# Performance work log

Hardware: AMD Instinct MI355X
Metric: run time of the kernel (lower is better)

Reference implementation:

```python
import jax, jax.numpy as jnp
from jax import lax
import numpy as np

V, D, H, E, L, B = 512, 128, 64, 4, 60, 4096
ADJ = 184  # ((180 + 7) // 8) * 8


def setup_inputs() -> dict:
    key = jax.random.key(0)
    it = iter(jax.random.split(key, 64))

    def nrm(shape, s=0.05):
        return jax.random.normal(next(it), shape, dtype=jnp.float32) * s

    x = jax.random.randint(next(it), (B, L), 0, V, dtype=jnp.int32)
    inp = {"x": x, "emb": nrm((V, D), 0.02).at[0].set(0.0)}  # padding_idx=0 row zero
    for d in ("f", "r"):
        inp[f"w_ih_{d}"] = nrm((4 * H, D)); inp[f"w_hh_{d}"] = nrm((4 * H, H))
        inp[f"b_ih_{d}"] = nrm((4 * H,)); inp[f"b_hh_{d}"] = nrm((4 * H,))
    for p, i_, h_, o_ in (("e", 1, 16, 8), ("l", 1, 16, 8), ("c", V, 32, 16), ("p", 6, 24, 12), ("x", 4, 16, 8)):
        inp[f"{p}_w1"] = nrm((h_, i_)); inp[f"{p}_b1"] = nrm((h_,))
        inp[f"{p}_w2"] = nrm((o_, h_)); inp[f"{p}_b2"] = nrm((o_,))
    inp["fp_w"] = nrm((ADJ, 180)); inp["fp_b"] = nrm((ADJ,))
    inp["attn_w"] = nrm((3 * ADJ, ADJ)); inp["attn_b"] = nrm((3 * ADJ,))
    inp["out_w"] = nrm((ADJ, ADJ)); inp["out_b"] = nrm((ADJ,))
    for i, (o_, i_) in enumerate(((128, ADJ), (64, 128), (32, 64), (E, 32)), 1):
        inp[f"g_w{i}"] = nrm((o_, i_)); inp[f"g_b{i}"] = nrm((o_,))
    return inp


def _mlp2(h, w1, b1, w2, b2):
    return jnp.maximum(h @ w1.T + b1, 0.0) @ w2.T + b2


def _lstm_final(xe, w_ih, w_hh, b_ih, b_hh):
    # torch LSTM gate order i, f, g, o; returns final hidden state [B, H]
    xg = jnp.einsum('bld,gd->blg', xe, w_ih) + b_ih
    h0 = jnp.zeros((xe.shape[0], H), xe.dtype)

    def step(carry, g_t):
        h, c = carry
        g = g_t + h @ w_hh.T + b_hh
        i, f, gg, o = jnp.split(g, 4, axis=-1)
        c = jax.nn.sigmoid(f) * c + jax.nn.sigmoid(i) * jnp.tanh(gg)
        h = jax.nn.sigmoid(o) * jnp.tanh(c)
        return (h, c), None

    (h, _), _ = lax.scan(step, (h0, h0), jnp.swapaxes(xg, 0, 1))
    return h


def _sequence_stats(x):
    # Fully vectorized equivalent of the per-sequence python loops
    f32 = jnp.float32
    mask = x != 0
    vlen = mask.sum(1)                                       # [B]
    vlenf = jnp.maximum(vlen, 1).astype(f32)
    pos = jnp.arange(L)
    # per-row histogram over valid tokens (torch.bincount of valid_seq)
    counts = jnp.zeros((B, V), f32).at[jnp.arange(B)[:, None], x].add(mask.astype(f32))
    probs = counts / jnp.maximum(counts.sum(1, keepdims=True), 1.0)
    entropy = -jnp.sum(probs * jnp.log(probs + 1e-8), axis=1)
    entropy = jnp.where(vlen > 1, entropy, 0.0)
    char_dist = counts / vlenf[:, None]
    # compact valid tokens to the front (torch: seq[seq != 0]), stable argsort
    order = jnp.argsort((~mask).astype(jnp.int32), axis=1)
    cseq = jnp.take_along_axis(x, order, axis=1)
    cseq = jnp.where(pos[None] < vlen[:, None], cseq, 0)
    a, b = cseq[:, :-1], cseq[:, 1:]
    pairmask = pos[: L - 1][None] < (vlen - 1)[:, None]
    den1 = jnp.maximum(vlen - 1, 1).astype(f32)
    repeat = ((a == b) & pairmask).sum(1) / den1
    inc = ((b > a) & pairmask).sum(1) / den1
    dec = ((b < a) & pairmask).sum(1) / den1
    m2 = pos[: L - 2][None] < (vlen - 2)[:, None]
    per = ((cseq[:, :-2] == cseq[:, 2:]) & m2).sum(1) / jnp.maximum(vlen - 2, 1)
    per = jnp.where(vlen >= 4, per, 0.0)
    diversity = (counts > 0).sum(1) / vlenf
    # longest run of equal consecutive tokens via cummax of reset positions
    eq = jnp.concatenate([jnp.zeros((B, 1), bool), (cseq[:, 1:] == cseq[:, :-1]) & (pos[1:][None] < vlen[:, None])], 1)
    lastreset = lax.cummax(jnp.where(eq, -1, pos[None]), axis=1)
    runlen = pos[None] - lastreset + 1
    max_rep = jnp.where(pos[None] < vlen[:, None], runlen, 0).max(1) / vlenf
    pattern = jnp.stack([repeat, inc, dec, per, diversity, max_rep], 1).astype(f32)
    pattern = jnp.where((vlen > 1)[:, None], pattern, 0.0)
    # unique bigrams: sort pair codes, count distinct valid codes
    codes = jnp.where(pairmask, a * V + b, -1)
    s = jnp.sort(codes, axis=1)
    prevc = jnp.concatenate([jnp.full((B, 1), -2, s.dtype), s[:, :-1]], 1)
    comp_ratio = ((s != prevc) & (s >= 0)).sum(1) / den1
    info_density = entropy / jnp.log(jnp.maximum(vlen, 2).astype(f32))
    # local complexity: mean over sliding windows of (#unique / w), w = min(5, len//2)
    wsel = jnp.minimum(5, vlen // 2)
    local = jnp.zeros((B,), f32)
    for w in (2, 3, 4, 5):
        nwin = L - w + 1
        sh = [cseq[:, k:k + nwin] for k in range(w)]
        u = jnp.ones((B, nwin), f32)
        for k in range(1, w):
            isnew = jnp.ones((B, nwin), bool)
            for m in range(k):
                isnew = isnew & (sh[k] != sh[m])
            u = u + isnew
        winmask = pos[:nwin][None] < (vlen - w + 1)[:, None]
        lc = (u * winmask).sum(1) / w / jnp.maximum(vlen - w + 1, 1)
        local = jnp.where(wsel == w, lc, local)
    trans = 1.0 - repeat  # transitions/(len-1) == 1 - repeat_ratio
    complexity = jnp.stack([comp_ratio, info_density, local, trans], 1).astype(f32)
    complexity = jnp.where((vlen > 1)[:, None], complexity, 0.0)
    return entropy, vlen, char_dist, pattern, complexity


def reference(x, emb, w_ih_f, w_hh_f, b_ih_f, b_hh_f, w_ih_r, w_hh_r, b_ih_r, b_hh_r, e_w1, e_b1, e_w2, e_b2, l_w1, l_b1, l_w2, l_b2, c_w1, c_b1, c_w2, c_b2, p_w1, p_b1, p_w2, p_b2, x_w1, x_b1, x_w2, x_b2, fp_w, fp_b, attn_w, attn_b, out_w, out_b, g_w1, g_b1, g_w2, g_b2, g_w3, g_b3, g_w4, g_b4):
    entropy, vlen, char_dist, pattern, complexity = _sequence_stats(x)
    xe = emb[x]                                               # [B, L, D]
    h_f = _lstm_final(xe, w_ih_f, w_hh_f, b_ih_f, b_hh_f)
    h_r = _lstm_final(xe[:, ::-1], w_ih_r, w_hh_r, b_ih_r, b_hh_r)
    feats = jnp.concatenate([
        h_f, h_r,
        _mlp2((entropy / 4.0)[:, None], e_w1, e_b1, e_w2, e_b2),
        _mlp2((vlen.astype(jnp.float32) / 60.0)[:, None], l_w1, l_b1, l_w2, l_b2),
        _mlp2(char_dist, c_w1, c_b1, c_w2, c_b2),
        _mlp2(pattern, p_w1, p_b1, p_w2, p_b2),
        _mlp2(complexity, x_w1, x_b1, x_w2, x_b2),
    ], axis=1)                                                # [B, 180]
    f = feats @ fp_w.T + fp_b                                 # [B, 184]
    # MultiheadAttention with seq_len == 1: softmax over a single key is 1,
    # so attended = out_proj(v_proj(f)) exactly (q/k projections cancel).
    wv, bv = attn_w[2 * ADJ:], attn_b[2 * ADJ:]
    attended = (f @ wv.T + bv) @ out_w.T + out_b
    h = jnp.maximum(attended @ g_w1.T + g_b1, 0.0)
    h = jnp.maximum(h @ g_w2.T + g_b2, 0.0)
    h = jnp.maximum(h @ g_w3.T + g_b3, 0.0)
    logits = h @ g_w4.T + g_b4
    return jax.nn.softmax(logits, axis=-1)  # eval path (training=False)
```

## Files before the change

### kernel.cpp

```cpp
#include <hip/hip_runtime.h>

#define BATCH 4096
#define SEQL  60
#define VOC   512
#define EMBD  128
#define HID   64
#define GATES 256
#define ADJ   184

typedef __attribute__((ext_vector_type(8))) short short8;
typedef __attribute__((ext_vector_type(4))) float f32x4;
typedef __attribute__((ext_vector_type(4))) unsigned short u16x4;

#define L2E  1.4426950408889634f
#define L2E2 2.8853900817779268f

__device__ __forceinline__ float ex2(float x) {
#if __has_builtin(__builtin_amdgcn_exp2f)
  return __builtin_amdgcn_exp2f(x);
#else
  return exp2f(x);
#endif
}
__device__ __forceinline__ unsigned short f2bf_rne(float f) {
  unsigned int u = __float_as_uint(f);
  unsigned int r = (u + 0x7fffu + ((u >> 16) & 1u)) >> 16;
  return (unsigned short)r;
}
__device__ __forceinline__ unsigned short f2bf(float f) {
  return (unsigned short)((__float_as_uint(f) + 0x8000u) >> 16);
}
__device__ __forceinline__ float dot4(float4 a, float4 b, float acc) {
  acc = fmaf(a.x, b.x, acc); acc = fmaf(a.y, b.y, acc);
  acc = fmaf(a.z, b.z, acc); acc = fmaf(a.w, b.w, acc);
  return acc;
}
__device__ __forceinline__ float wsumf(float v) {
  #pragma unroll
  for (int s = 32; s > 0; s >>= 1) v += __shfl_xor(v, s, 64);
  return v;
}
__device__ __forceinline__ int wsumi(int v) {
  #pragma unroll
  for (int s = 32; s > 0; s >>= 1) v += __shfl_xor(v, s, 64);
  return v;
}
__device__ __forceinline__ int wmaxi(int v) {
  #pragma unroll
  for (int s = 32; s > 0; s >>= 1) v = max(v, __shfl_xor(v, s, 64));
  return v;
}

__global__ __launch_bounds__(256) void k_prep(
    const int* __restrict__ x,
    const float* __restrict__ emb,
    const float* __restrict__ wih_f, const float* __restrict__ bif, const float* __restrict__ bhf,
    const float* __restrict__ wih_r, const float* __restrict__ bir, const float* __restrict__ bhr,
    const float* __restrict__ whh_f, const float* __restrict__ whh_r,
    const float* __restrict__ g_w1, const float* __restrict__ g_b1,
    const float* __restrict__ out_w, const float* __restrict__ out_b,
    const float* __restrict__ attn_w, const float* __restrict__ attn_b,
    const float* __restrict__ fp_w, const float* __restrict__ fp_b,
    const float* __restrict__ g_w2, const float* __restrict__ g_w3,
    const float* __restrict__ g_w4, const float* __restrict__ c_w1,
    float* __restrict__ G_f, float* __restrict__ G_r,
    unsigned short* __restrict__ Wfrag,
    float* __restrict__ A, float* __restrict__ avb,
    float* __restrict__ Bp, float* __restrict__ vb,
    float* __restrict__ g_w2t, float* __restrict__ g_w3t, float* __restrict__ g_w4t,
    float* __restrict__ c_w1t,
    float* __restrict__ ent_o, float* __restrict__ vlen_o,
    float* __restrict__ pat_o, float* __restrict__ cpx_o) {
  __shared__ unsigned int cnt[4][512];
  __shared__ unsigned short q[4][68];
  const int bid = blockIdx.x;
  const int tid = threadIdx.x;

  if (bid < 128) {
    const int dir = bid >> 6;
    const int rem = bid & 63;
    const int v0 = (rem >> 2) * 32;
    const int j0 = (rem & 3) * 64;
    const float* W = dir ? wih_r : wih_f;
    const float* bi = dir ? bir : bif;
    const float* bh = dir ? bhr : bhf;
    float* G = dir ? G_r : G_f;
    const int vp = tid >> 4;
    const int jq = tid & 15;
    const int v = v0 + vp * 2;
    const int j = j0 + jq * 4;
    const int gg = j >> 6;
    const int u0 = j & 63;
    const float sc = (gg == 2) ? L2E2 : L2E;

    const float4* E0 = (const float4*)(emb + (size_t)v * 128);
    const float4* E1 = (const float4*)(emb + (size_t)(v + 1) * 128);
    const float4* W0 = (const float4*)(W + (size_t)j * 128);
    const float4* W1 = (const float4*)(W + (size_t)(j + 1) * 128);
    const float4* W2 = (const float4*)(W + (size_t)(j + 2) * 128);
    const float4* W3 = (const float4*)(W + (size_t)(j + 3) * 128);

    float a00 = 0.f, a01 = 0.f, a02 = 0.f, a03 = 0.f;
    float a10 = 0.f, a11 = 0.f, a12 = 0.f, a13 = 0.f;
    #pragma unroll 4
    for (int d4 = 0; d4 < 32; d4++) {
      float4 e0 = E0[d4], e1 = E1[d4];
      float4 w0 = W0[d4], w1 = W1[d4], w2 = W2[d4], w3 = W3[d4];
      a00 = dot4(e0, w0, a00); a01 = dot4(e0, w1, a01);
      a02 = dot4(e0, w2, a02); a03 = dot4(e0, w3, a03);
      a10 = dot4(e1, w0, a10); a11 = dot4(e1, w1, a11);
      a12 = dot4(e1, w2, a12); a13 = dot4(e1, w3, a13);
    }
    float b0v = bi[j] + bh[j], b1v = bi[j + 1] + bh[j + 1];
    float b2v = bi[j + 2] + bh[j + 2], b3v = bi[j + 3] + bh[j + 3];
    float* g0 = G + (size_t)v * 256 + u0 * 4 + gg;
    g0[0]  = (a00 + b0v) * sc; g0[4]  = (a01 + b1v) * sc;
    g0[8]  = (a02 + b2v) * sc; g0[12] = (a03 + b3v) * sc;
    float* g1 = g0 + 256;
    g1[0]  = (a10 + b0v) * sc; g1[4]  = (a11 + b1v) * sc;
    g1[8]  = (a12 + b2v) * sc; g1[12] = (a13 + b3v) * sc;
  } else if (bid < 144) {
    const int id = (bid - 128) * 256 + tid;
    const int lane = id & 63;
    const int fc = id >> 6;
    const int c = fc & 1;
    const int gg = (fc >> 1) & 3;
    const int w = (fc >> 3) & 3;
    const int dir = fc >> 5;
    const float* whh = dir ? whh_r : whh_f;
    const float sc = (gg == 2) ? L2E2 : L2E;
    const int n = gg * 64 + w * 16 + (lane & 15);
    const int kb = c * 32 + (lane >> 4) * 8;
    unsigned short* o = Wfrag + (size_t)id * 8;
    #pragma unroll
    for (int j = 0; j < 8; j++) o[j] = f2bf_rne(whh[n * 64 + kb + j] * sc);
  } else if (bid < 272) {
    const int i = bid - 144;
    const int j = tid;
    const float* g1r = g_w1 + (size_t)i * ADJ;
    if (j < ADJ) {
      float a0 = 0.f, a1 = 0.f, a2 = 0.f, a3 = 0.f;
      for (int k = 0; k < ADJ; k += 4) {
        a0 = fmaf(g1r[k],     out_w[(size_t)(k)     * ADJ + j], a0);
        a1 = fmaf(g1r[k + 1], out_w[(size_t)(k + 1) * ADJ + j], a1);
        a2 = fmaf(g1r[k + 2], out_w[(size_t)(k + 2) * ADJ + j], a2);
        a3 = fmaf(g1r[k + 3], out_w[(size_t)(k + 3) * ADJ + j], a3);
      }
      A[(size_t)i * ADJ + j] = (a0 + a1) + (a2 + a3);
    } else if (j == ADJ) {
      float a0 = 0.f;
      for (int k = 0; k < ADJ; k++) a0 = fmaf(g1r[k], out_b[k], a0);
      avb[i] = a0 + g_b1[i];
    }
  } else if (bid < 456) {
    const int k = bid - 272;
    const int j = tid;
    const float* wvr = attn_w + (size_t)(2 * ADJ + k) * ADJ;
    if (j < 180) {
      float a0 = 0.f, a1 = 0.f, a2 = 0.f, a3 = 0.f;
      for (int m = 0; m < ADJ; m += 4) {
        a0 = fmaf(wvr[m],     fp_w[(size_t)(m)     * 180 + j], a0);
        a1 = fmaf(wvr[m + 1], fp_w[(size_t)(m + 1) * 180 + j], a1);
        a2 = fmaf(wvr[m + 2], fp_w[(size_t)(m + 2) * 180 + j], a2);
        a3 = fmaf(wvr[m + 3], fp_w[(size_t)(m + 3) * 180 + j], a3);
      }
      Bp[(size_t)k * 180 + j] = (a0 + a1) + (a2 + a3);
    } else if (j == 180) {
      float a0 = 0.f;
      for (int m = 0; m < ADJ; m++) a0 = fmaf(wvr[m], fp_b[m], a0);
      vb[k] = a0 + attn_b[2 * ADJ + k];
    }
  } else if (bid == 456) {
    for (int i = tid; i < 64 * 128; i += 256) {
      int o = i >> 7, k = i & 127;
      g_w2t[k * 64 + o] = g_w2[i];
    }
    for (int i = tid; i < 32 * 64; i += 256) {
      int o = i >> 6, k = i & 63;
      g_w3t[k * 32 + o] = g_w3[i];
    }
    if (tid < 128) {
      int o = tid >> 5, k = tid & 31;
      g_w4t[k * 4 + o] = g_w4[tid];
    }
  } else if (bid < 465) {
    const int base = (bid - 457) * 2048;
    for (int i = tid; i < 2048; i += 256) {
      int idx = base + i;
      int o = idx >> 9, k = idx & 511;
      c_w1t[k * 32 + o] = k ? c_w1[o * 512 + k] : 0.f;
    }
  } else {
    const int lane = tid & 63;
    const int wid = tid >> 6;
    const int row = (bid - 465) * 4 + wid;
    unsigned int* cr = cnt[wid];
    unsigned short* qr = q[wid];

    for (int i = lane; i < 512; i += 64) cr[i] = 0u;
    qr[lane] = 0;
    if (lane < 4) qr[64 + lane] = 0;
    int v = (lane < 60) ? x[row * 60 + lane] : 0;
    bool act = (v != 0);
    unsigned long long amask = __ballot(act);
    int n = __popcll(amask);
    __syncthreads();
    if (act) {
      int pos = __popcll(amask & ((1ull << lane) - 1ull));
      qr[pos] = (unsigned short)v;
      atomicAdd(&cr[v], 1u);
    }
    __syncthreads();

    float vlenf = (float)(n >= 1 ? n : 1);
    float inv = 1.f / vlenf;

    float ent = 0.f; int distinct = 0;
    #pragma unroll
    for (int j = 0; j < 8; j++) {
      unsigned int c = cr[lane + j * 64];
      if (c) {
        distinct++;
        float p = (float)c * inv;
        ent -= p * __logf(p + 1e-8f);
      }
    }
    ent = wsumf(ent);
    distinct = wsumi(distinct);

    int a = qr[lane], b = qr[lane + 1], c2 = qr[lane + 2];
    bool v1 = (lane + 1 < n);
    bool v2 = (lane + 2 < n);
    int rep  = __popcll(__ballot(v1 && (a == b)));
    int incs = __popcll(__ballot(v1 && (b > a)));
    int decs = __popcll(__ballot(v1 && (b < a)));
    int per2 = __popcll(__ballot(v2 && (a == c2)));

    int prev = (lane > 0) ? (int)qr[lane - 1] : -1;
    bool isst = (lane < n) && (lane == 0 || a != prev);
    unsigned long long smask = __ballot(isst);
    int len = 0;
    if (isst) {
      unsigned long long hi = (lane < 63) ? (smask >> (lane + 1)) : 0ull;
      int next = hi ? (lane + __ffsll((unsigned long long)hi)) : n;
      len = next - lane;
    }
    int maxrun = wmaxi(len);

    int code = v1 ? (a * VOC + b) : -1;
    int unique = v1 ? 1 : 0;
    #pragma unroll 1
    for (int j = 0; j < 58; j++) {
      int cj = __shfl(code, j, 64);
      if (j < lane && cj == code) unique = 0;
    }
    int dc = __popcll(__ballot(unique != 0));

    int wl = n >> 1; if (wl > 5) wl = 5;
    float local = 0.f;
    if (wl >= 2) {
      bool pv = (lane + wl <= n);
      int u = 0;
      if (pv) {
        int t0 = qr[lane], t1 = qr[lane + 1], t2 = qr[lane + 2];
        int t3 = qr[lane + 3], t4 = qr[lane + 4];
        u = 1;
        u += (t1 != t0);
        if (wl >= 3) u += (int)((t2 != t1) && (t2 != t0));
        if (wl >= 4) u += (int)((t3 != t2) && (t3 != t1) && (t3 != t0));
        if (wl >= 5) u += (int)((t4 != t3) && (t4 != t2) && (t4 != t1) && (t4 != t0));
      }
      int usum = wsumi(u);
      int denw = n - wl + 1; if (denw < 1) denw = 1;
      local = (float)usum / (float)wl / (float)denw;
    }

    float den1 = (float)((n - 1) >= 1 ? (n - 1) : 1);
    float repeat = (float)rep / den1;
    float per = (n >= 4) ? (float)per2 / (float)((n - 2) >= 1 ? (n - 2) : 1) : 0.f;
    float entz = (n > 1) ? ent : 0.f;
    float z = (n > 1) ? 1.f : 0.f;

    if (lane == 0) {
      ent_o[row] = entz;
      vlen_o[row] = (float)n;
      pat_o[row * 6 + 0] = repeat * z;
      pat_o[row * 6 + 1] = (float)incs / den1 * z;
      pat_o[row * 6 + 2] = (float)decs / den1 * z;
      pat_o[row * 6 + 3] = per * z;
      pat_o[row * 6 + 4] = (float)distinct * inv * z;
      pat_o[row * 6 + 5] = (float)maxrun * inv * z;
      cpx_o[row * 4 + 0] = (float)dc / den1 * z;
      cpx_o[row * 4 + 1] = entz / __logf((float)(n >= 2 ? n : 2)) * z;
      cpx_o[row * 4 + 2] = local * z;
      cpx_o[row * 4 + 3] = (1.f - repeat) * z;
    }
  }
}

#define LSTM_BAR()                                                             \
  do {                                                                         \
    asm volatile("s_waitcnt lgkmcnt(0)" ::: "memory");                         \
    __builtin_amdgcn_s_barrier();                                              \
    __builtin_amdgcn_sched_barrier(0);                                         \
  } while (0)

#define LSTM_STEP(T, CUR, NXT)                                                 \
  {                                                                            \
    const unsigned short* hb = hbuf[(T) & 1];                                  \
    short8 hf0 = *(const short8*)(hb + rdoff);                                 \
    short8 hf1 = *(const short8*)(hb + rdoff + 32);                            \
    if ((T) < 59) {                                                            \
      int tsn = dir ? (58 - (T)) : ((T) + 1);                                  \
      const char* gp = Gb2 + tokoff[tsn * 16 + ln];                            \
      NXT[0] = *(const float4*)(gp);                                           \
      NXT[1] = *(const float4*)(gp + 16);                                      \
      NXT[2] = *(const float4*)(gp + 32);                                      \
      NXT[3] = *(const float4*)(gp + 48);                                      \
    }                                                                          \
    f32x4 z0 = {0.f, 0.f, 0.f, 0.f};                                           \
    f32x4 acc0 = z0, acc1 = z0, acc2 = z0, acc3 = z0;                          \
    acc0 = __builtin_amdgcn_mfma_f32_16x16x32_bf16(bfr[0][0], hf0, acc0, 0, 0, 0); \
    acc1 = __builtin_amdgcn_mfma_f32_16x16x32_bf16(bfr[1][0], hf0, acc1, 0, 0, 0); \
    acc2 = __builtin_amdgcn_mfma_f32_16x16x32_bf16(bfr[2][0], hf0, acc2, 0, 0, 0); \
    acc3 = __builtin_amdgcn_mfma_f32_16x16x32_bf16(bfr[3][0], hf0, acc3, 0, 0, 0); \
    acc0 = __builtin_amdgcn_mfma_f32_16x16x32_bf16(bfr[0][1], hf1, acc0, 0, 0, 0); \
    acc1 = __builtin_amdgcn_mfma_f32_16x16x32_bf16(bfr[1][1], hf1, acc1, 0, 0, 0); \
    acc2 = __builtin_amdgcn_mfma_f32_16x16x32_bf16(bfr[2][1], hf1, acc2, 0, 0, 0); \
    acc3 = __builtin_amdgcn_mfma_f32_16x16x32_bf16(bfr[3][1], hf1, acc3, 0, 0, 0); \
    unsigned short* hw = hbuf[((T) + 1) & 1];                                  \
    unsigned short hh[4];                                                      \
    _Pragma("unroll")                                                          \
    for (int r = 0; r < 4; r++) {                                              \
      float gi = acc0[r] + CUR[r].x;                                           \
      float gf = acc1[r] + CUR[r].y;                                           \
      float gc = acc2[r] + CUR[r].z;                                           \
      float go = acc3[r] + CUR[r].w;                                           \
      float Ef = ex2(-gf);                                                     \
      float E1 = ex2(-gi);                                                     \
      float E2 = ex2(gc);                                                      \
      float sf = __builtin_amdgcn_rcpf(1.f + Ef);                              \
      float p  = (E2 - 1.f) * __builtin_amdgcn_rcpf((1.f + E1) * (E2 + 1.f));  \
      float cn = fmaf(sf, cst[r], p);                                          \
      cst[r] = cn;                                                             \
      float E3 = ex2(-go);                                                     \
      float E4 = ex2(fminf(L2E2 * cn, 126.f));                                 \
      float h  = (E4 - 1.f) * __builtin_amdgcn_rcpf((1.f + E3) * (E4 + 1.f));  \
      hv[r] = h;                                                               \
      hh[r] = f2bf(h);                                                         \
    }                                                                          \
    u16x4 hvv = {hh[0], hh[1], hh[2], hh[3]};                                  \
    *(u16x4*)(hw + wroff) = hvv;                                               \
    if ((T) == 59) {                                                           \
      float4 o4; o4.x = hv[0]; o4.y = hv[1]; o4.z = hv[2]; o4.w = hv[3];       \
      *(float4*)(hop) = o4;                                                    \
    }                                                                          \
    LSTM_BAR();                                                                \
  }

__global__ __launch_bounds__(256) void k_main(
    const int* __restrict__ x,
    const float* __restrict__ G_f, const float* __restrict__ G_r,
    const unsigned short* __restrict__ Wfrag,
    const float* __restrict__ A, const float* __restrict__ avb,
    const float* __restrict__ Bp, const float* __restrict__ vb,
    float* __restrict__ C1t, float* __restrict__ c1b,
    float* __restrict__ hf_o, float* __restrict__ hr_o) {
  __shared__ __align__(16) unsigned short hbuf[2][16 * 72];
  __shared__ __align__(16) unsigned int tokoff[60 * 16];
  const int bid = blockIdx.x;
  const int tid = threadIdx.x;

  if (bid < 512) {
    const int lane = tid & 63;
    const int w = tid >> 6;
    const int dir = bid >> 8;
    const int blk = bid & 255;
    const int b0 = blk << 4;
    const float* G = dir ? G_r : G_f;
    float* ho = dir ? hr_o : hf_o;

    for (int i = tid; i < 960; i += 256) {
      int r = i / 60, t = i - r * 60;
      tokoff[t * 16 + r] = ((unsigned int)x[(size_t)(b0 + r) * 60 + t]) << 10;
    }
    for (int i = tid; i < 16 * 72; i += 256) hbuf[0][i] = 0;

    short8 bfr[4][2];
    #pragma unroll
    for (int gg = 0; gg < 4; gg++)
      #pragma unroll
      for (int c = 0; c < 2; c++) {
        int idx = (((dir * 4 + w) * 4 + gg) * 2 + c) * 64 + lane;
        bfr[gg][c] = *(const short8*)(Wfrag + (size_t)idx * 8);
      }

    const int kg = lane >> 4;
    const int ln = lane & 15;
    const int ub2 = w * 16 + kg * 4;
    const int rdoff = ln * 72 + kg * 8;
    const int wroff = ln * 72 + ub2;
    const char* Gb2 = (const char*)G + (size_t)ub2 * 16;
    float* hop = ho + (size_t)(b0 + ln) * 64 + ub2;
    float cst[4] = {0.f, 0.f, 0.f, 0.f};
    float4 gvA[4], gvB[4];
    float hv[4];

    __syncthreads();

    {
      int ts0 = dir ? 59 : 0;
      const char* gp = Gb2 + tokoff[ts0 * 16 + ln];
      gvA[0] = *(const float4*)(gp);
      gvA[1] = *(const float4*)(gp + 16);
      gvA[2] = *(const float4*)(gp + 32);
      gvA[3] = *(const float4*)(gp + 48);
    }

    #pragma unroll 1
    for (int tt = 0; tt < 30; tt++) {
      const int t0 = tt * 2, t1 = tt * 2 + 1;
      LSTM_STEP(t0, gvA, gvB)
      LSTM_STEP(t1, gvB, gvA)
    }
  } else {
    const int i = bid - 512, j = tid;
    const float* Ar = A + (size_t)i * ADJ;
    if (j < 180) {
      float a0 = 0.f, a1 = 0.f, a2 = 0.f, a3 = 0.f;
      for (int k = 0; k < ADJ; k += 4) {
        a0 = fmaf(Ar[k],     Bp[(size_t)(k)     * 180 + j], a0);
        a1 = fmaf(Ar[k + 1], Bp[(size_t)(k + 1) * 180 + j], a1);
        a2 = fmaf(Ar[k + 2], Bp[(size_t)(k + 2) * 180 + j], a2);
        a3 = fmaf(Ar[k + 3], Bp[(size_t)(k + 3) * 180 + j], a3);
      }
      C1t[(size_t)j * 128 + i] = (a0 + a1) + (a2 + a3);
    } else if (j == 180) {
      float a0 = 0.f;
      for (int k = 0; k < ADJ; k++) a0 = fmaf(Ar[k], vb[k], a0);
      c1b[i] = a0 + avb[i];
    }
  }
}

#define FSTR 192

__global__ __launch_bounds__(256) void k_head(
    const int* __restrict__ x,
    const float* __restrict__ hf, const float* __restrict__ hr,
    const float* __restrict__ ent, const float* __restrict__ vlen,
    const float* __restrict__ pat, const float* __restrict__ cpx,
    const float* __restrict__ e_w1, const float* __restrict__ e_b1,
    const float* __restrict__ e_w2, const float* __restrict__ e_b2,
    const float* __restrict__ l_w1, const float* __restrict__ l_b1,
    const float* __restrict__ l_w2, const float* __restrict__ l_b2,
    const float* __restrict__ c_w1t, const float* __restrict__ c_b1,
    const float* __restrict__ c_w2, const float* __restrict__ c_b2,
    const float* __restrict__ p_w1, const float* __restrict__ p_b1,
    const float* __restrict__ p_w2, const float* __restrict__ p_b2,
    const float* __restrict__ x_w1, const float* __restrict__ x_b1,
    const float* __restrict__ x_w2, const float* __restrict__ x_b2,
    const float* __restrict__ C1t, const float* __restrict__ c1b,
    const float* __restrict__ g_w2t, const float* __restrict__ g_b2,
    const float* __restrict__ g_w3t, const float* __restrict__ g_b3,
    const float* __restrict__ g_w4t, const float* __restrict__ g_b4,
    float* __restrict__ out) {
  __shared__ float feat[8 * FSTR];
  __shared__ unsigned short tk[8 * 64];
  __shared__ float h1[8 * 128];
  __shared__ float h2[8 * 64];
  __shared__ float h3[8 * 32];
  __shared__ float h1c[8 * 33];
  __shared__ float lg[32];
  const int tid = threadIdx.x;
  const int b0 = blockIdx.x * 8;

  if (tid < 128) {
    int r = tid >> 4, c = tid & 15;
    float4 vv = ((const float4*)(hf + (size_t)(b0 + r) * 64))[c];
    *(float4*)(feat + r * FSTR + c * 4) = vv;
  } else {
    int t = tid - 128;
    int r = t >> 4, c = t & 15;
    float4 vv = ((const float4*)(hr + (size_t)(b0 + r) * 64))[c];
    *(float4*)(feat + r * FSTR + 64 + c * 4) = vv;
  }
  for (int i = tid; i < 480; i += 256) {
    int r = i / 60, t = i - r * 60;
    tk[r * 64 + t] = (unsigned short)x[(size_t)(b0 + r) * 60 + t];
  }
  __syncthreads();
  {
    int o = tid & 31, r = tid >> 5;
    const unsigned short* tkr = tk + r * 64;
    float a0 = 0.f, a1 = 0.f, a2 = 0.f, a3 = 0.f;
    #pragma unroll 5
    for (int t = 0; t < 60; t += 4) {
      int t0 = tkr[t], t1 = tkr[t + 1], t2 = tkr[t + 2], t3 = tkr[t + 3];
      a0 += c_w1t[t0 * 32 + o];
      a1 += c_w1t[t1 * 32 + o];
      a2 += c_w1t[t2 * 32 + o];
      a3 += c_w1t[t3 * 32 + o];
    }
    float invv = __builtin_amdgcn_rcpf(fmaxf(vlen[b0 + r], 1.f));
    h1c[r * 33 + o] = fmaxf(((a0 + a1) + (a2 + a3)) * invv + c_b1[o], 0.f);
  }
  __syncthreads();
  if (tid < 32) {
    const int m = tid & 3, r = tid >> 2, b = b0 + r;
    float tt[24];
    if (m == 0) {
      float ein = ent[b] * 0.25f;
      #pragma unroll
      for (int o = 0; o < 16; o++) tt[o] = fmaxf(e_w1[o] * ein + e_b1[o], 0.f);
      #pragma unroll
      for (int o = 0; o < 8; o++) {
        float a = e_b2[o];
        #pragma unroll
        for (int k = 0; k < 16; k++) a = fmaf(e_w2[o * 16 + k], tt[k], a);
        feat[r * FSTR + 128 + o] = a;
      }
    } else if (m == 1) {
      float lin = vlen[b] * (1.f / 60.f);
      #pragma unroll
      for (int o = 0; o < 16; o++) tt[o] = fmaxf(l_w1[o] * lin + l_b1[o], 0.f);
      #pragma unroll
      for (int o = 0; o < 8; o++) {
        float a = l_b2[o];
        #pragma unroll
        for (int k = 0; k < 16; k++) a = fmaf(l_w2[o * 16 + k], tt[k], a);
        feat[r * FSTR + 136 + o] = a;
      }
    } else if (m == 2) {
      float pin[6];
      #pragma unroll
      for (int k = 0; k < 6; k++) pin[k] = pat[b * 6 + k];
      #pragma unroll
      for (int o = 0; o < 24; o++) {
        float a = p_b1[o];
        #pragma unroll
        for (int k = 0; k < 6; k++) a = fmaf(p_w1[o * 6 + k], pin[k], a);
        tt[o] = fmaxf(a, 0.f);
      }
      #pragma unroll
      for (int o = 0; o < 12; o++) {
        float a = p_b2[o];
        #pragma unroll
        for (int k = 0; k < 24; k++) a = fmaf(p_w2[o * 24 + k], tt[k], a);
        feat[r * FSTR + 160 + o] = a;
      }
    } else {
      float xin[4];
      #pragma unroll
      for (int k = 0; k < 4; k++) xin[k] = cpx[b * 4 + k];
      #pragma unroll
      for (int o = 0; o < 16; o++) {
        float a = x_b1[o];
        #pragma unroll
        for (int k = 0; k < 4; k++) a = fmaf(x_w1[o * 4 + k], xin[k], a);
        tt[o] = fmaxf(a, 0.f);
      }
      #pragma unroll
      for (int o = 0; o < 8; o++) {
        float a = x_b2[o];
        #pragma unroll
        for (int k = 0; k < 16; k++) a = fmaf(x_w2[o * 16 + k], tt[k], a);
        feat[r * FSTR + 172 + o] = a;
      }
    }
  } else if (tid >= 64 && tid < 192) {
    int t = tid - 64;
    int r = t >> 4, o = t & 15;
    float a = c_b2[o];
    const float* hh = h1c + r * 33;
    #pragma unroll
    for (int k = 0; k < 32; k++) a = fmaf(c_w2[o * 32 + k], hh[k], a);
    feat[r * FSTR + 144 + o] = a;
  }
  __syncthreads();

  {
    const int o = tid & 127, rg = tid >> 7;
    const float* f0p = feat + (rg * 4 + 0) * FSTR;
    const float* f1p = feat + (rg * 4 + 1) * FSTR;
    const float* f2p = feat + (rg * 4 + 2) * FSTR;
    const float* f3p = feat + (rg * 4 + 3) * FSTR;
    float a0 = 0.f, a1 = 0.f, a2 = 0.f, a3 = 0.f;
    #pragma unroll 3
    for (int k4 = 0; k4 < 45; k4++) {
      float w0 = C1t[(size_t)(k4 * 4 + 0) * 128 + o];
      float w1 = C1t[(size_t)(k4 * 4 + 1) * 128 + o];
      float w2 = C1t[(size_t)(k4 * 4 + 2) * 128 + o];
      float w3 = C1t[(size_t)(k4 * 4 + 3) * 128 + o];
      float4 f0 = *(const float4*)(f0p + k4 * 4);
      float4 f1 = *(const float4*)(f1p + k4 * 4);
      float4 f2 = *(const float4*)(f2p + k4 * 4);
      float4 f3 = *(const float4*)(f3p + k4 * 4);
      a0 = fmaf(w0, f0.x, a0); a0 = fmaf(w1, f0.y, a0);
      a0 = fmaf(w2, f0.z, a0); a0 = fmaf(w3, f0.w, a0);
      a1 = fmaf(w0, f1.x, a1); a1 = fmaf(w1, f1.y, a1);
      a1 = fmaf(w2, f1.z, a1); a1 = fmaf(w3, f1.w, a1);
      a2 = fmaf(w0, f2.x, a2); a2 = fmaf(w1, f2.y, a2);
      a2 = fmaf(w2, f2.z, a2); a2 = fmaf(w3, f2.w, a2);
      a3 = fmaf(w0, f3.x, a3); a3 = fmaf(w1, f3.y, a3);
      a3 = fmaf(w2, f3.z, a3); a3 = fmaf(w3, f3.w, a3);
    }
    float bb = c1b[o];
    h1[(rg * 4 + 0) * 128 + o] = fmaxf(a0 + bb, 0.f);
    h1[(rg * 4 + 1) * 128 + o] = fmaxf(a1 + bb, 0.f);
    h1[(rg * 4 + 2) * 128 + o] = fmaxf(a2 + bb, 0.f);
    h1[(rg * 4 + 3) * 128 + o] = fmaxf(a3 + bb, 0.f);
  }
  __syncthreads();
  {
    const int o = tid & 63, rg = tid >> 6;
    const float* f0p = h1 + (rg * 2 + 0) * 128;
    const float* f1p = h1 + (rg * 2 + 1) * 128;
    float a0 = 0.f, a1 = 0.f;
    #pragma unroll 4
    for (int k4 = 0; k4 < 32; k4++) {
      float w0 = g_w2t[(k4 * 4 + 0) * 64 + o];
      float w1 = g_w2t[(k4 * 4 + 1) * 64 + o];
      float w2 = g_w2t[(k4 * 4 + 2) * 64 + o];
      float w3 = g_w2t[(k4 * 4 + 3) * 64 + o];
      float4 f0 = *(const float4*)(f0p + k4 * 4);
      float4 f1 = *(const float4*)(f1p + k4 * 4);
      a0 = fmaf(w0, f0.x, a0); a0 = fmaf(w1, f0.y, a0);
      a0 = fmaf(w2, f0.z, a0); a0 = fmaf(w3, f0.w, a0);
      a1 = fmaf(w0, f1.x, a1); a1 = fmaf(w1, f1.y, a1);
      a1 = fmaf(w2, f1.z, a1); a1 = fmaf(w3, f1.w, a1);
    }
    float bb = g_b2[o];
    h2[(rg * 2 + 0) * 64 + o] = fmaxf(a0 + bb, 0.f);
    h2[(rg * 2 + 1) * 64 + o] = fmaxf(a1 + bb, 0.f);
  }
  __syncthreads();
  {
    const int o = tid & 31, rg = tid >> 5;
    const float* fp = h2 + rg * 64;
    float a = 0.f;
    #pragma unroll 4
    for (int k4 = 0; k4 < 16; k4++) {
      float w0 = g_w3t[(k4 * 4 + 0) * 32 + o];
      float w1 = g_w3t[(k4 * 4 + 1) * 32 + o];
      float w2 = g_w3t[(k4 * 4 + 2) * 32 + o];
      float w3 = g_w3t[(k4 * 4 + 3) * 32 + o];
      float4 f0 = *(const float4*)(fp + k4 * 4);
      a = fmaf(w0, f0.x, a); a = fmaf(w1, f0.y, a);
      a = fmaf(w2, f0.z, a); a = fmaf(w3, f0.w, a);
    }
    h3[rg * 32 + o] = fmaxf(a + g_b3[o], 0.f);
  }
  __syncthreads();
  if (tid < 32) {
    int r = tid >> 2, o = tid & 3;
    const float* hh = h3 + r * 32;
    float a = g_b4[o];
    #pragma unroll
    for (int k = 0; k < 32; k++) a = fmaf(g_w4t[k * 4 + o], hh[k], a);
    lg[tid] = a;
  }
  __syncthreads();
  if (tid < 8) {
    float l0 = lg[tid * 4 + 0], l1 = lg[tid * 4 + 1];
    float l2 = lg[tid * 4 + 2], l3 = lg[tid * 4 + 3];
    float m = fmaxf(fmaxf(l0, l1), fmaxf(l2, l3));
    float e0 = __expf(l0 - m), e1 = __expf(l1 - m);
    float e2 = __expf(l2 - m), e3 = __expf(l3 - m);
    float is = __builtin_amdgcn_rcpf(e0 + e1 + e2 + e3);
    float4 o4; o4.x = e0 * is; o4.y = e1 * is; o4.z = e2 * is; o4.w = e3 * is;
    *(float4*)(out + (size_t)(b0 + tid) * 4) = o4;
  }
}

extern "C" void kernel_launch(void* const* d_in, const int* in_sizes, int n_in,
                              void* d_out, int out_size, void* d_ws, size_t ws_size,
                              hipStream_t stream) {
  const int*   x     = (const int*)d_in[0];
  const float* emb   = (const float*)d_in[1];
  const float* wih_f = (const float*)d_in[2];
  const float* whh_f = (const float*)d_in[3];
  const float* bih_f = (const float*)d_in[4];
  const float* bhh_f = (const float*)d_in[5];
  const float* wih_r = (const float*)d_in[6];
  const float* whh_r = (const float*)d_in[7];
  const float* bih_r = (const float*)d_in[8];
  const float* bhh_r = (const float*)d_in[9];
  const float* e_w1 = (const float*)d_in[10]; const float* e_b1 = (const float*)d_in[11];
  const float* e_w2 = (const float*)d_in[12]; const float* e_b2 = (const float*)d_in[13];
  const float* l_w1 = (const float*)d_in[14]; const float* l_b1 = (const float*)d_in[15];
  const float* l_w2 = (const float*)d_in[16]; const float* l_b2 = (const float*)d_in[17];
  const float* c_w1 = (const float*)d_in[18]; const float* c_b1 = (const float*)d_in[19];
  const float* c_w2 = (const float*)d_in[20]; const float* c_b2 = (const float*)d_in[21];
  const float* p_w1 = (const float*)d_in[22]; const float* p_b1 = (const float*)d_in[23];
  const float* p_w2 = (const float*)d_in[24]; const float* p_b2 = (const float*)d_in[25];
  const float* x_w1 = (const float*)d_in[26]; const float* x_b1 = (const float*)d_in[27];
  const float* x_w2 = (const float*)d_in[28]; const float* x_b2 = (const float*)d_in[29];
  const float* fp_w = (const float*)d_in[30]; const float* fp_b = (const float*)d_in[31];
  const float* attn_w = (const float*)d_in[32]; const float* attn_b = (const float*)d_in[33];
  const float* out_w = (const float*)d_in[34]; const float* out_b = (const float*)d_in[35];
  const float* g_w1 = (const float*)d_in[36]; const float* g_b1 = (const float*)d_in[37];
  const float* g_w2 = (const float*)d_in[38]; const float* g_b2 = (const float*)d_in[39];
  const float* g_w3 = (const float*)d_in[40]; const float* g_b3 = (const float*)d_in[41];
  const float* g_w4 = (const float*)d_in[42]; const float* g_b4 = (const float*)d_in[43];

  float* ws   = (float*)d_ws;
  float* G_f  = ws;
  float* G_r  = G_f  + 512 * 256;
  float* hfw  = G_r  + 512 * 256;
  float* hrw  = hfw  + BATCH * 64;
  float* entw = hrw  + BATCH * 64;
  float* vlnw = entw + BATCH;
  float* patw = vlnw + BATCH;
  float* cpxw = patw + BATCH * 6;
  float* Aw   = cpxw + BATCH * 4;
  float* avbw = Aw + 128 * ADJ;
  float* Bpw  = avbw + 128;
  float* vbw  = Bpw + ADJ * 180;
  float* C1t  = vbw + ADJ;
  float* c1b  = C1t + 180 * 128;
  float* g2t  = c1b + 128;
  float* g3t  = g2t + 128 * 64;
  float* g4t  = g3t + 64 * 32;
  float* cw1t = g4t + 32 * 4;
  unsigned short* Wfrag = (unsigned short*)(cw1t + 512 * 32);

  k_prep<<<dim3(465 + BATCH / 4), dim3(256), 0, stream>>>(
      x, emb, wih_f, bih_f, bhh_f, wih_r, bih_r, bhh_r, whh_f, whh_r,
      g_w1, g_b1, out_w, out_b, attn_w, attn_b, fp_w, fp_b,
      g_w2, g_w3, g_w4, c_w1,
      G_f, G_r, Wfrag, Aw, avbw, Bpw, vbw, g2t, g3t, g4t, cw1t,
      entw, vlnw, patw, cpxw);
  k_main<<<dim3(640), dim3(256), 0, stream>>>(
      x, G_f, G_r, Wfrag, Aw, avbw, Bpw, vbw, C1t, c1b, hfw, hrw);
  k_head<<<dim3(BATCH / 8), dim3(256), 0, stream>>>(
      x, hfw, hrw, entw, vlnw, patw, cpxw,
      e_w1, e_b1, e_w2, e_b2, l_w1, l_b1, l_w2, l_b2,
      cw1t, c_b1, c_w2, c_b2, p_w1, p_b1, p_w2, p_b2,
      x_w1, x_b1, x_w2, x_b2, C1t, c1b,
      g2t, g_b2, g3t, g_b3, g4t, g_b4,
      (float*)d_out);
}
```

Baseline: 250.2 us.

## Stage LSTM input-gate rows into LDS via async global_load_lds double buffer

Replaces the per-lane register prefetch of the next timestep's precomputed input-gate rows with async global-to-LDS loads (global_load_lds, 16 bytes per lane), double-buffered in shared memory. Each wave fetches whole 1KB token rows coalesced, and lanes then read their gate slices from LDS. The custom lgkmcnt barrier becomes __syncthreads, which also waits on vmcnt, so the loads of the next step must finish before each step's barrier. That can stall the serial recurrence on global latency, and the change also raises LDS use.

```diff
diff --git a/kernel.cpp b/kernel.cpp
--- a/kernel.cpp
+++ b/kernel.cpp
@@ -15,6 +15,8 @@
 #define L2E  1.4426950408889634f
 #define L2E2 2.8853900817779268f
 
+#define GROW 1040
+
 __device__ __forceinline__ float ex2(float x) {
 #if __has_builtin(__builtin_amdgcn_exp2f)
   return __builtin_amdgcn_exp2f(x);
@@ -49,6 +51,11 @@
   #pragma unroll
   for (int s = 32; s > 0; s >>= 1) v = max(v, __shfl_xor(v, s, 64));
   return v;
+}
+__device__ __forceinline__ void gload16(const void* g, void* l) {
+  __builtin_amdgcn_global_load_lds(
+      (const __attribute__((address_space(1))) void*)g,
+      (__attribute__((address_space(3))) void*)l, 16, 0, 0);
 }
 
 __global__ __launch_bounds__(256) void k_prep(
@@ -298,26 +305,26 @@
   }
 }
 
-#define LSTM_BAR()                                                             \
-  do {                                                                         \
-    asm volatile("s_waitcnt lgkmcnt(0)" ::: "memory");                         \
-    __builtin_amdgcn_s_barrier();                                              \
-    __builtin_amdgcn_sched_barrier(0);                                         \
-  } while (0)
-
-#define LSTM_STEP(T, CUR, NXT)                                                 \
+#define LSTM_STEP(T)                                                           \
   {                                                                            \
+    if ((T) < 59) {                                                            \
+      const int tsn = dir ? (58 - (T)) : ((T) + 1);                            \
+      const unsigned int* toks = tokoff + tsn * 16;                            \
+      char* gdst = Gm + (((T) + 1) & 1) * (16 * GROW) + r4 * GROW;             \
+      gload16(GbC + toks[r4 + 0] + lane16, gdst);                              \
+      gload16(GbC + toks[r4 + 1] + lane16, gdst + GROW);                       \
+      gload16(GbC + toks[r4 + 2] + lane16, gdst + 2 * GROW);                   \
+      gload16(GbC + toks[r4 + 3] + lane16, gdst + 3 * GROW);                   \
+    }                                                                          \
     const unsigned short* hb = hbuf[(T) & 1];                                  \
     short8 hf0 = *(const short8*)(hb + rdoff);                                 \
     short8 hf1 = *(const short8*)(hb + rdoff + 32);                            \
-    if ((T) < 59) {                                                            \
-      int tsn = dir ? (58 - (T)) : ((T) + 1);                                  \
-      const char* gp = Gb2 + tokoff[tsn * 16 + ln];                            \
-      NXT[0] = *(const float4*)(gp);                                           \
-      NXT[1] = *(const float4*)(gp + 16);                                      \
-      NXT[2] = *(const float4*)(gp + 32);                                      \
-      NXT[3] = *(const float4*)(gp + 48);                                      \
-    }                                                                          \
+    const char* gbp = Gm + ((T) & 1) * (16 * GROW) + goff;                     \
+    float4 gvv[4];                                                             \
+    gvv[0] = *(const float4*)(gbp);                                            \
+    gvv[1] = *(const float4*)(gbp + 16);                                       \
+    gvv[2] = *(const float4*)(gbp + 32);                                       \
+    gvv[3] = *(const float4*)(gbp + 48);                                       \
     f32x4 z0 = {0.f, 0.f, 0.f, 0.f};                                           \
     f32x4 acc0 = z0, acc1 = z0, acc2 = z0, acc3 = z0;                          \
     acc0 = __builtin_amdgcn_mfma_f32_16x16x32_bf16(bfr[0][0], hf0, acc0, 0, 0, 0); \
@@ -330,12 +337,13 @@
     acc3 = __builtin_amdgcn_mfma_f32_16x16x32_bf16(bfr[3][1], hf1, acc3, 0, 0, 0); \
     unsigned short* hw = hbuf[((T) + 1) & 1];                                  \
     unsigned short hh[4];                                                      \
+    float hv[4];                                                               \
     _Pragma("unroll")                                                          \
     for (int r = 0; r < 4; r++) {                                              \
-      float gi = acc0[r] + CUR[r].x;                                           \
-      float gf = acc1[r] + CUR[r].y;                                           \
-      float gc = acc2[r] + CUR[r].z;                                           \
-      float go = acc3[r] + CUR[r].w;                                           \
+      float gi = acc0[r] + gvv[r].x;                                           \
+      float gf = acc1[r] + gvv[r].y;                                           \
+      float gc = acc2[r] + gvv[r].z;                                           \
+      float go = acc3[r] + gvv[r].w;                                           \
       float Ef = ex2(-gf);                                                     \
       float E1 = ex2(-gi);                                                     \
       float E2 = ex2(gc);                                                      \
@@ -355,7 +363,7 @@
       float4 o4; o4.x = hv[0]; o4.y = hv[1]; o4.z = hv[2]; o4.w = hv[3];       \
       *(float4*)(hop) = o4;                                                    \
     }                                                                          \
-    LSTM_BAR();                                                                \
+    __syncthreads();                                                           \
   }
 
 __global__ __launch_bounds__(256) void k_main(
@@ -366,6 +374,7 @@
     const float* __restrict__ Bp, const float* __restrict__ vb,
     float* __restrict__ C1t, float* __restrict__ c1b,
     float* __restrict__ hf_o, float* __restrict__ hr_o) {
+  __shared__ __align__(16) char Gm[2 * 16 * GROW];
   __shared__ __align__(16) unsigned short hbuf[2][16 * 72];
   __shared__ __align__(16) unsigned int tokoff[60 * 16];
   const int bid = blockIdx.x;
@@ -378,6 +387,7 @@
     const int blk = bid & 255;
     const int b0 = blk << 4;
     const float* G = dir ? G_r : G_f;
+    const char* GbC = (const char*)G;
     float* ho = dir ? hr_o : hf_o;
 
     for (int i = tid; i < 960; i += 256) {
@@ -400,28 +410,30 @@
     const int ub2 = w * 16 + kg * 4;
     const int rdoff = ln * 72 + kg * 8;
     const int wroff = ln * 72 + ub2;
-    const char* Gb2 = (const char*)G + (size_t)ub2 * 16;
+    const int r4 = w * 4;
+    const int lane16 = lane * 16;
+    const int goff = ln * GROW + ub2 * 16;
     float* hop = ho + (size_t)(b0 + ln) * 64 + ub2;
     float cst[4] = {0.f, 0.f, 0.f, 0.f};
-    float4 gvA[4], gvB[4];
-    float hv[4];
 
     __syncthreads();
 
     {
-      int ts0 = dir ? 59 : 0;
-      const char* gp = Gb2 + tokoff[ts0 * 16 + ln];
-      gvA[0] = *(const float4*)(gp);
-      gvA[1] = *(const float4*)(gp + 16);
-      gvA[2] = *(const float4*)(gp + 32);
-      gvA[3] = *(const float4*)(gp + 48);
-    }
+      const int ts0 = dir ? 59 : 0;
+      const unsigned int* toks = tokoff + ts0 * 16;
+      char* gdst = Gm + r4 * GROW;
+      gload16(GbC + toks[r4 + 0] + lane16, gdst);
+      gload16(GbC + toks[r4 + 1] + lane16, gdst + GROW);
+      gload16(GbC + toks[r4 + 2] + lane16, gdst + 2 * GROW);
+      gload16(GbC + toks[r4 + 3] + lane16, gdst + 3 * GROW);
+    }
+    __syncthreads();
 
     #pragma unroll 1
     for (int tt = 0; tt < 30; tt++) {
       const int t0 = tt * 2, t1 = tt * 2 + 1;
-      LSTM_STEP(t0, gvA, gvB)
-      LSTM_STEP(t1, gvB, gvA)
+      LSTM_STEP(t0)
+      LSTM_STEP(t1)
     }
   } else {
     const int i = bid - 512, j = tid;
```

New measurement: 246.2 us. About the same (-1.6%).
